# Optimization experiments

Measured on AMD Instinct MI355X. Metric: run time of the kernel, lower is better.

Reference implementation:

```python
import jax, jax.numpy as jnp
import numpy as np


def setup_inputs() -> dict:
    key = jax.random.key(0)
    x = jax.random.normal(key, (1024, 65536), dtype=jnp.float32)
    return {"x": x, "k": 64}


def reference(x, k):
    # BatchTopK: ReLU, then keep the k*batch largest activations across the
    # ENTIRE flattened batch, zeroing everything else.
    acts = jax.nn.relu(x)
    flat = acts.reshape(-1)                      # [batch * d_sae]
    k_total = k * x.shape[0]
    vals, idx = jax.lax.top_k(flat, k_total)     # global selection
    out = jnp.zeros_like(flat).at[idx].set(vals) # scatter back
    return out.reshape(acts.shape)
```

## Files before the change

kernel.cpp:

```cpp
#include <hip/hip_runtime.h>
#include <stdint.h>


#define HDR_CURSOR 0
#define HDR_FLAG   1
#define HDR_THR    2
#define HDR_ICUT   3
#define HIST_OFF   4096
#define CAND_OFF   16384
#define NBINS      2048u
#define BUCKET_CAP 6144u
#define SCAN_STAGE 1024
#define ROWS       1024u
#define SPEC       3.0f
#define BASE_BITS  0x40400000u

__device__ __forceinline__ uint32_t bin_of(uint32_t key) {
  uint32_t off = key - BASE_BITS;
  uint32_t b = off >> 12;
  return b < NBINS ? b : (NBINS - 1u);
}

__device__ __forceinline__ float max4(float4 a) {
  return fmaxf(fmaxf(a.x, a.y), fmaxf(a.z, a.w));
}

__global__ void k_init(uint32_t* hdr, uint32_t* ghist, uint32_t force_flag) {
  for (uint32_t i = threadIdx.x; i < 64u + NBINS; i += 256u) {
    if (i < 64u) hdr[i] = 0u;
    else ghist[i - 64u] = 0u;
  }
  if (threadIdx.x == 0u) hdr[HDR_FLAG] = force_flag;
}

__device__ __forceinline__ void push4(float4 a, uint32_t gi,
                                      uint32_t* s_cnt, uint2* s_buf) {
  if (a.x >= SPEC) { uint32_t p = atomicAdd(s_cnt, 1u); if (p < SCAN_STAGE) s_buf[p] = make_uint2(__float_as_uint(a.x), gi); }
  if (a.y >= SPEC) { uint32_t p = atomicAdd(s_cnt, 1u); if (p < SCAN_STAGE) s_buf[p] = make_uint2(__float_as_uint(a.y), gi + 1u); }
  if (a.z >= SPEC) { uint32_t p = atomicAdd(s_cnt, 1u); if (p < SCAN_STAGE) s_buf[p] = make_uint2(__float_as_uint(a.z), gi + 2u); }
  if (a.w >= SPEC) { uint32_t p = atomicAdd(s_cnt, 1u); if (p < SCAN_STAGE) s_buf[p] = make_uint2(__float_as_uint(a.w), gi + 3u); }
}

__global__ __launch_bounds__(256) void k_scan(
    const float4* __restrict__ x4, const float* __restrict__ x,
    uint2* __restrict__ cand, uint32_t* __restrict__ hdr,
    uint32_t* __restrict__ ghist,
    uint32_t cap, uint32_t n4, uint32_t n) {
  __shared__ uint32_t s_cnt;
  __shared__ uint32_t s_base;
  __shared__ uint2 s_buf[SCAN_STAGE];
  uint32_t tid = threadIdx.x;
  if (tid == 0u) s_cnt = 0u;
  __syncthreads();

  uint32_t lane = tid & 63u;
  uint32_t gwid = (blockIdx.x * blockDim.x + tid) >> 6;
  uint32_t nw   = (gridDim.x * blockDim.x) >> 6;
  uint32_t nchunk = n4 >> 8;
  for (uint32_t c = gwid; c < nchunk; c += nw) {
    uint32_t base = c << 8;
    float4 a0 = x4[base + lane];
    float4 a1 = x4[base + 64u + lane];
    float4 a2 = x4[base + 128u + lane];
    float4 a3 = x4[base + 192u + lane];
    if (__ballot(max4(a0) >= SPEC)) push4(a0, (base + lane) * 4u, &s_cnt, s_buf);
    if (__ballot(max4(a1) >= SPEC)) push4(a1, (base + 64u + lane) * 4u, &s_cnt, s_buf);
    if (__ballot(max4(a2) >= SPEC)) push4(a2, (base + 128u + lane) * 4u, &s_cnt, s_buf);
    if (__ballot(max4(a3) >= SPEC)) push4(a3, (base + 192u + lane) * 4u, &s_cnt, s_buf);
  }
  uint32_t rem0 = nchunk << 8;
  if (blockIdx.x == 0u) {
    for (uint32_t i = rem0 + tid; i < n4; i += blockDim.x) {
      float4 a = x4[i];
      if (__ballot(max4(a) >= SPEC)) push4(a, i * 4u, &s_cnt, s_buf);
    }
    uint32_t tail0 = n4 * 4u;
    if (tid < (n - tail0)) {
      uint32_t gi = tail0 + tid;
      float v = x[gi];
      if (v >= SPEC) { uint32_t p = atomicAdd(&s_cnt, 1u); if (p < SCAN_STAGE) s_buf[p] = make_uint2(__float_as_uint(v), gi); }
    }
  }
  __syncthreads();
  uint32_t cnt = s_cnt;
  if (cnt == 0u) return;
  uint32_t wcnt = cnt < (uint32_t)SCAN_STAGE ? cnt : (uint32_t)SCAN_STAGE;
  if (tid == 0u) {
    s_base = atomicAdd(&hdr[HDR_CURSOR], cnt);
    if (cnt > (uint32_t)SCAN_STAGE) atomicOr(&hdr[HDR_FLAG], 1u);
  }
  __syncthreads();
  uint32_t base = s_base;
  for (uint32_t j = tid; j < wcnt; j += blockDim.x) {
    uint32_t gidx = base + j;
    if (gidx < cap) {
      uint2 c = s_buf[j];
      cand[gidx] = c;
      atomicAdd(&ghist[bin_of(c.x)], 1u);
    }
  }
  if (tid == 0u && base + wcnt > cap) atomicOr(&hdr[HDR_FLAG], 1u);
}

__global__ __launch_bounds__(1024) void k_finish(
    const uint2* __restrict__ cand, uint32_t* __restrict__ hdr,
    const uint32_t* __restrict__ ghist, const int* __restrict__ kptr,
    const float* __restrict__ x, float* __restrict__ out,
    uint32_t cap, uint32_t n) {
  __shared__ __align__(16) uint8_t smem[57344];
  uint32_t* h      = (uint32_t*)smem;
  uint2*    bkt    = (uint2*)(smem + 8192);
  uint32_t* eq_idx = (uint32_t*)(smem + 8192);
  __shared__ uint32_t s_sel, s_rank, s_bcnt, s_need, s_found, s_eqcnt, s_icut;
  uint32_t tid = threadIdx.x;
  uint32_t K = (uint32_t)kptr[0] * ROWS;
  uint32_t M = hdr[HDR_CURSOR];
  if (tid == 0u) s_need = 0u;
  __syncthreads();

  bool skip_sel = (hdr[HDR_FLAG] != 0u || M > cap || M < K);
  if (skip_sel) {
    if (tid == 0u) s_need = 1u;
  } else if (K == 0u) {
    if (tid == 0u) { hdr[HDR_THR] = 0xFFFFFFFFu; hdr[HDR_ICUT] = 0xFFFFFFFFu; }
    return;
  } else {
    h[tid] = ghist[tid];
    h[tid + 1024u] = ghist[tid + 1024u];
    if (tid == 0u) s_bcnt = 0u;
    __syncthreads();
    if (tid < 64u) {
      uint32_t seg = NBINS >> 6;
      uint32_t base = tid * seg;
      uint32_t lanesum = 0u;
      for (uint32_t j = 0; j < seg; ++j) lanesum += h[base + j];
      uint32_t s = lanesum;
      for (int d = 1; d < 64; d <<= 1) {
        uint32_t v = (uint32_t)__shfl_down((int)s, d, 64);
        if ((int)tid + d < 64) s += v;
      }
      uint32_t above = s - lanesum;
      if (above < K && above + lanesum >= K) {
        uint32_t r = K - above;
        uint32_t cum = 0u;
        for (int j = (int)seg - 1; j >= 0; --j) {
          uint32_t c = h[base + (uint32_t)j];
          if (cum + c >= r) { s_sel = base + (uint32_t)j; s_rank = r - cum; break; }
          cum += c;
        }
      }
    }
    __syncthreads();
    uint32_t bsel = s_sel;
    uint32_t r = s_rank;
    uint32_t E = h[bsel];
    if (bsel == NBINS - 1u || E > BUCKET_CAP) {
      if (tid == 0u) s_need = 1u;
    } else {
      const uint4* __restrict__ cand4 = (const uint4*)cand;
      uint32_t M2 = M >> 1;
      uint32_t j = tid;
      for (; j + 3072u < M2; j += 4096u) {
        uint4 c0 = cand4[j];
        uint4 c1 = cand4[j + 1024u];
        uint4 c2 = cand4[j + 2048u];
        uint4 c3 = cand4[j + 3072u];
        if (bin_of(c0.x) == bsel) { uint32_t p = atomicAdd(&s_bcnt, 1u); if (p < BUCKET_CAP) bkt[p] = make_uint2(c0.x, c0.y); }
        if (bin_of(c0.z) == bsel) { uint32_t p = atomicAdd(&s_bcnt, 1u); if (p < BUCKET_CAP) bkt[p] = make_uint2(c0.z, c0.w); }
        if (bin_of(c1.x) == bsel) { uint32_t p = atomicAdd(&s_bcnt, 1u); if (p < BUCKET_CAP) bkt[p] = make_uint2(c1.x, c1.y); }
        if (bin_of(c1.z) == bsel) { uint32_t p = atomicAdd(&s_bcnt, 1u); if (p < BUCKET_CAP) bkt[p] = make_uint2(c1.z, c1.w); }
        if (bin_of(c2.x) == bsel) { uint32_t p = atomicAdd(&s_bcnt, 1u); if (p < BUCKET_CAP) bkt[p] = make_uint2(c2.x, c2.y); }
        if (bin_of(c2.z) == bsel) { uint32_t p = atomicAdd(&s_bcnt, 1u); if (p < BUCKET_CAP) bkt[p] = make_uint2(c2.z, c2.w); }
        if (bin_of(c3.x) == bsel) { uint32_t p = atomicAdd(&s_bcnt, 1u); if (p < BUCKET_CAP) bkt[p] = make_uint2(c3.x, c3.y); }
        if (bin_of(c3.z) == bsel) { uint32_t p = atomicAdd(&s_bcnt, 1u); if (p < BUCKET_CAP) bkt[p] = make_uint2(c3.z, c3.w); }
      }
      for (; j < M2; j += 1024u) {
        uint4 c = cand4[j];
        if (bin_of(c.x) == bsel) { uint32_t p = atomicAdd(&s_bcnt, 1u); if (p < BUCKET_CAP) bkt[p] = make_uint2(c.x, c.y); }
        if (bin_of(c.z) == bsel) { uint32_t p = atomicAdd(&s_bcnt, 1u); if (p < BUCKET_CAP) bkt[p] = make_uint2(c.z, c.w); }
      }
      if (tid == 0u && (M & 1u)) {
        uint2 c = cand[M - 1u];
        if (bin_of(c.x) == bsel) { uint32_t p = atomicAdd(&s_bcnt, 1u); if (p < BUCKET_CAP) bkt[p] = c; }
      }
      __syncthreads();
      for (uint32_t e = tid; e < E; e += 1024u) {
        uint2 me = bkt[e];
        uint32_t rank = 0u;
        for (uint32_t jj = 0; jj < E; ++jj) {
          uint2 o = bkt[jj];
          rank += (o.x > me.x || (o.x == me.x && o.y < me.y)) ? 1u : 0u;
        }
        if (rank == r - 1u) { hdr[HDR_THR] = me.x; hdr[HDR_ICUT] = me.y; }
      }
    }
  }
  __syncthreads();
  if (s_need == 0u) return;
  if (tid == 0u) hdr[HDR_FLAG] = 1u;

  uint32_t prefix = 0u;
  uint32_t R = K;
  bool zero_thr = (K == 0u);
  for (int lvl = 0; lvl < 3 && !zero_thr; ++lvl) {
    uint32_t shift = (lvl == 0) ? 21u : (lvl == 1 ? 10u : 0u);
    uint32_t nb = (lvl == 2) ? 1024u : 2048u;
    for (uint32_t b = tid; b < nb; b += 1024u) h[b] = 0u;
    __syncthreads();
    for (uint32_t i = tid; i < n; i += 1024u) {
      float v = x[i];
      uint32_t key = (v > 0.f) ? __float_as_uint(v) : 0u;
      bool valid = (key != 0u);
      if (lvl == 1) valid = valid && ((key >> 21) == prefix);
      if (lvl == 2) valid = valid && ((key >> 10) == prefix);
      if (valid) atomicAdd(&h[(key >> shift) & (nb - 1u)], 1u);
    }
    __syncthreads();
    if (tid == 0u) {
      uint32_t cum = 0u, sel = 0u, rr = R, found = 0u;
      for (int b = (int)nb - 1; b >= 0; --b) {
        uint32_t c = h[b];
        if (cum + c >= R) { sel = (uint32_t)b; rr = R - cum; found = 1u; break; }
        cum += c;
      }
      s_sel = sel; s_rank = rr; s_found = found;
    }
    __syncthreads();
    if (s_found == 0u) {
      zero_thr = true;
    } else {
      uint32_t sel = s_sel;
      R = s_rank;
      if (lvl == 0) prefix = sel;
      else if (lvl == 1) prefix = (prefix << 11) | sel;
      else prefix = (prefix << 10) | sel;
    }
    __syncthreads();
  }
  uint32_t thr_key = zero_thr ? 0u : prefix;
  uint32_t icut = 0xFFFFFFFFu;
  if (!zero_thr) {
    uint32_t E2 = h[thr_key & 1023u];
    uint32_t T = R;
    if (T < E2) {
      if (tid == 0u) { s_eqcnt = 0u; s_icut = 0xFFFFFFFFu; }
      __syncthreads();
      for (uint32_t i = tid; i < n; i += 1024u) {
        float v = x[i];
        if (v > 0.f && __float_as_uint(v) == thr_key) {
          uint32_t p = atomicAdd(&s_eqcnt, 1u);
          if (p < 4096u) eq_idx[p] = i;
        }
      }
      __syncthreads();
      uint32_t ec = s_eqcnt < 4096u ? s_eqcnt : 4096u;
      for (uint32_t e = tid; e < ec; e += 1024u) {
        uint32_t me = eq_idx[e];
        uint32_t rank = 0u;
        for (uint32_t j = 0; j < ec; ++j) rank += (eq_idx[j] < me) ? 1u : 0u;
        if (rank == T - 1u) s_icut = me;
      }
      __syncthreads();
      icut = s_icut;
    }
  }
  for (uint32_t i = tid; i < n; i += 1024u) {
    float v = x[i];
    uint32_t key = (v > 0.f) ? __float_as_uint(v) : 0u;
    bool keep = (key > thr_key) || (key != 0u && key == thr_key && i <= icut);
    out[i] = keep ? v : 0.f;
  }
}

__global__ __launch_bounds__(256) void k_scatter(
    const uint2* __restrict__ cand, const uint32_t* __restrict__ hdr,
    float* __restrict__ out, uint32_t cap) {
  if (hdr[HDR_FLAG] != 0u) return;
  uint32_t M = hdr[HDR_CURSOR]; if (M > cap) M = cap;
  uint32_t thr = hdr[HDR_THR], icut = hdr[HDR_ICUT];
  uint32_t stride = gridDim.x * blockDim.x;
  for (uint32_t i = blockIdx.x * blockDim.x + threadIdx.x; i < M; i += stride) {
    uint2 c = cand[i];
    if (c.x > thr || (c.x == thr && c.y <= icut)) out[c.y] = __uint_as_float(c.x);
  }
}

extern "C" void kernel_launch(void* const* d_in, const int* in_sizes, int n_in,
                              void* d_out, int out_size, void* d_ws, size_t ws_size,
                              hipStream_t stream) {
  const float* x = (const float*)d_in[0];
  const int* kptr = (const int*)d_in[1];
  float* out = (float*)d_out;
  uint32_t n = (uint32_t)in_sizes[0];
  uint32_t n4 = n >> 2;

  uint32_t* hdr = (uint32_t*)d_ws;
  uint32_t* ghist = (uint32_t*)((char*)d_ws + HIST_OFF);
  uint2* cand = (uint2*)((char*)d_ws + CAND_OFF);
  uint32_t cap = (ws_size > (size_t)CAND_OFF) ? (uint32_t)((ws_size - CAND_OFF) / 8) : 0u;

  if (cap < 131072u) {
    k_init<<<1, 256, 0, stream>>>(hdr, ghist, 1u);
  } else {
    hipMemsetAsync(d_ws, 0, 12288, stream);
  }
  k_scan<<<2048, 256, 0, stream>>>((const float4*)x, x, cand, hdr, ghist, cap, n4, n);
  hipMemsetAsync(out, 0, (size_t)n * 4u, stream);
  k_finish<<<1, 1024, 0, stream>>>(cand, hdr, ghist, kptr, x, out, cap, n);
  k_scatter<<<512, 256, 0, stream>>>(cand, hdr, out, cap);
}
```

Before: 484.8 us.

## Fuse output zeroing into scan kernel via interleaved block roles

Replaces the separate hipMemsetAsync of the output with a combined kernel in which alternating groups of 8 blocks either zero the output or run the candidate scan. Reading x and writing zeros to out then run concurrently in one launch, which removes a launch and serialisation, but the scan now has half as many blocks and each group only gets part of the bandwidth. The last ballot predicate is also rewritten into an equivalent form.

```diff
diff --git a/kernel.cpp b/kernel.cpp
--- a/kernel.cpp
+++ b/kernel.cpp
@@ -41,21 +41,38 @@
   if (a.w >= SPEC) { uint32_t p = atomicAdd(s_cnt, 1u); if (p < SCAN_STAGE) s_buf[p] = make_uint2(__float_as_uint(a.w), gi + 3u); }
 }
 
-__global__ __launch_bounds__(256) void k_scan(
+__global__ __launch_bounds__(256) void k_scanzero(
+    float4* __restrict__ out4, float* __restrict__ out,
     const float4* __restrict__ x4, const float* __restrict__ x,
     uint2* __restrict__ cand, uint32_t* __restrict__ hdr,
     uint32_t* __restrict__ ghist,
-    uint32_t cap, uint32_t n4, uint32_t n) {
+    uint32_t cap, uint32_t n4, uint32_t n, uint32_t half) {
+  uint32_t g    = blockIdx.x >> 3;
+  uint32_t role = g & 1u;
+  uint32_t bid  = (g >> 1) * 8u + (blockIdx.x & 7u);
+  uint32_t tid  = threadIdx.x;
+  uint32_t tail0 = n4 * 4u;
+
+  if (role == 0u) {
+    const float4 z = make_float4(0.f, 0.f, 0.f, 0.f);
+    uint32_t stride = half * 256u;
+#pragma unroll 4
+    for (uint32_t i = bid * 256u + tid; i < n4; i += stride)
+      out4[i] = z;
+    if (bid == 0u && tid < (n - tail0))
+      out[tail0 + tid] = 0.f;
+    return;
+  }
+
   __shared__ uint32_t s_cnt;
   __shared__ uint32_t s_base;
   __shared__ uint2 s_buf[SCAN_STAGE];
-  uint32_t tid = threadIdx.x;
   if (tid == 0u) s_cnt = 0u;
   __syncthreads();
 
   uint32_t lane = tid & 63u;
-  uint32_t gwid = (blockIdx.x * blockDim.x + tid) >> 6;
-  uint32_t nw   = (gridDim.x * blockDim.x) >> 6;
+  uint32_t gwid = (bid * 256u + tid) >> 6;
+  uint32_t nw   = (half * 256u) >> 6;
   uint32_t nchunk = n4 >> 8;
   for (uint32_t c = gwid; c < nchunk; c += nw) {
     uint32_t base = c << 8;
@@ -66,15 +83,15 @@
     if (__ballot(max4(a0) >= SPEC)) push4(a0, (base + lane) * 4u, &s_cnt, s_buf);
     if (__ballot(max4(a1) >= SPEC)) push4(a1, (base + 64u + lane) * 4u, &s_cnt, s_buf);
     if (__ballot(max4(a2) >= SPEC)) push4(a2, (base + 128u + lane) * 4u, &s_cnt, s_buf);
-    if (__ballot(max4(a3) >= SPEC)) push4(a3, (base + 192u + lane) * 4u, &s_cnt, s_buf);
+    if (__ballot(a3.x >= SPEC || a3.y >= SPEC || a3.z >= SPEC || a3.w >= SPEC ? 1 : 0))
+      push4(a3, (base + 192u + lane) * 4u, &s_cnt, s_buf);
   }
   uint32_t rem0 = nchunk << 8;
-  if (blockIdx.x == 0u) {
-    for (uint32_t i = rem0 + tid; i < n4; i += blockDim.x) {
+  if (bid == 0u) {
+    for (uint32_t i = rem0 + tid; i < n4; i += 256u) {
       float4 a = x4[i];
       if (__ballot(max4(a) >= SPEC)) push4(a, i * 4u, &s_cnt, s_buf);
     }
-    uint32_t tail0 = n4 * 4u;
     if (tid < (n - tail0)) {
       uint32_t gi = tail0 + tid;
       float v = x[gi];
@@ -304,8 +321,9 @@
   } else {
     hipMemsetAsync(d_ws, 0, 12288, stream);
   }
-  k_scan<<<2048, 256, 0, stream>>>((const float4*)x, x, cand, hdr, ghist, cap, n4, n);
-  hipMemsetAsync(out, 0, (size_t)n * 4u, stream);
+  const uint32_t HALF = 1024u;
+  k_scanzero<<<2u * HALF, 256, 0, stream>>>((float4*)out, out, (const float4*)x, x,
+                                            cand, hdr, ghist, cap, n4, n, HALF);
   k_finish<<<1, 1024, 0, stream>>>(cand, hdr, ghist, kptr, x, out, cap, n);
   k_scatter<<<512, 256, 0, stream>>>(cand, hdr, out, cap);
 }
```

Result: slower. 494.6 us (+2.0%).
